# Performance work log

Measured on AMD Instinct MI355X. Metric: run time of the kernel, lower is better.

## Reference

```python
import jax, jax.numpy as jnp
import numpy as np

EPS = 1e-8
BOX2D_IDX = jnp.array([0, 1, 3, 4, 6])  # x, y, dx, dy, yaw


def box2corners(box):
    # box: (..., 5) = (x, y, w, h, alpha) -> corners (..., 4, 2), CCW order
    x, y, w, h, a = (box[..., i] for i in range(5))
    tx = jnp.array([0.5, -0.5, -0.5, 0.5], box.dtype)
    ty = jnp.array([0.5, 0.5, -0.5, -0.5], box.dtype)
    x4 = tx * w[..., None]
    y4 = ty * h[..., None]
    c, s = jnp.cos(a)[..., None], jnp.sin(a)[..., None]
    rx = c * x4 - s * y4 + x[..., None]
    ry = s * x4 + c * y4 + y[..., None]
    return jnp.stack([rx, ry], axis=-1)


def edge_intersections(c1, c2):
    # all 4x4 edge-edge intersections of two quads -> pts (..., 16, 2), mask (..., 16)
    p1 = c1[..., :, None, :]
    p2 = jnp.roll(c1, -1, axis=-2)[..., :, None, :]
    q1 = c2[..., None, :, :]
    q2 = jnp.roll(c2, -1, axis=-2)[..., None, :, :]
    r = p2 - p1
    s = q2 - q1
    denom = r[..., 0] * s[..., 1] - r[..., 1] * s[..., 0]
    safe = jnp.where(jnp.abs(denom) < EPS, 1.0, denom)
    qp = q1 - p1
    t = (qp[..., 0] * s[..., 1] - qp[..., 1] * s[..., 0]) / safe
    u = (qp[..., 0] * r[..., 1] - qp[..., 1] * r[..., 0]) / safe
    mask = (jnp.abs(denom) > EPS) & (t > 0) & (t < 1) & (u > 0) & (u < 1)
    pts = jnp.where(mask[..., None], p1 + t[..., None] * r, 0.0)
    lead = pts.shape[:-3]
    return pts.reshape(lead + (16, 2)), mask.reshape(lead + (16,))


def points_in_box(pts, corners):
    # pts (..., K, 2) inside rotated quad given by corners (..., 4, 2) -> (..., K) bool
    a = corners[..., 0:1, :]
    ab = corners[..., 1:2, :] - a
    ad = corners[..., 3:4, :] - a
    ap = pts - a
    pab = jnp.sum(ap * ab, -1)
    pad = jnp.sum(ap * ad, -1)
    nab = jnp.sum(ab * ab, -1)
    nad = jnp.sum(ad * ad, -1)
    return (pab > 0) & (pab < nab) & (pad > 0) & (pad < nad)


def masked_polygon_area(verts, mask):
    # verts (..., 24, 2) candidate vertices, mask (..., 24) validity
    m = mask.astype(verts.dtype)
    num = jnp.maximum(jnp.sum(m, -1, keepdims=True), 1.0)
    mean = jnp.sum(verts * m[..., None], -2, keepdims=True) / num[..., None]
    d = verts - mean  # centered (shoelace is translation-invariant)
    ang = jnp.arctan2(d[..., 1], d[..., 0])
    # push invalid vertices to the end with stable tie-break
    ang = jnp.where(mask, ang, 1e6 + jnp.arange(24, dtype=ang.dtype))
    idx = jnp.argsort(ang, axis=-1)
    vs = jnp.take_along_axis(d, idx[..., None], axis=-2)
    ms = jnp.take_along_axis(mask, idx, axis=-1)
    v0 = vs[..., 0:1, :]
    vs = jnp.where(ms[..., None], vs, v0)  # collapse invalid onto first vertex
    nxt = jnp.roll(vs, -1, axis=-2)
    cross = vs[..., 0] * nxt[..., 1] - vs[..., 1] * nxt[..., 0]
    return 0.5 * jnp.abs(jnp.sum(cross, -1))


def rotated_iou_3d(b1, b2):
    # b1, b2: (..., 7) = (x, y, z, dx, dy, dz, yaw); elementwise-aligned IoU
    c1 = box2corners(b1[..., BOX2D_IDX])
    c2 = box2corners(b2[..., BOX2D_IDX])
    ipts, imask = edge_intersections(c1, c2)
    in1 = points_in_box(c1, c2)
    in2 = points_in_box(c2, c1)
    verts = jnp.concatenate([c1, c2, ipts], axis=-2)  # (..., 24, 2)
    mask = jnp.concatenate([in1, in2, imask], axis=-1)
    inter2d = masked_polygon_area(verts, mask)
    zmax = jnp.minimum(b1[..., 2] + 0.5 * b1[..., 5], b2[..., 2] + 0.5 * b2[..., 5])
    zmin = jnp.maximum(b1[..., 2] - 0.5 * b1[..., 5], b2[..., 2] - 0.5 * b2[..., 5])
    inter3d = inter2d * jnp.maximum(zmax - zmin, 0.0)
    v1 = b1[..., 3] * b1[..., 4] * b1[..., 5]
    v2 = b2[..., 3] * b2[..., 4] * b2[..., 5]
    return inter3d / (v1 + v2 - inter3d + EPS)


def setup_inputs() -> dict:
    key = jax.random.key(0)
    k1, k2, k3, k4, k5 = jax.random.split(key, 5)
    N = 1048576
    ctr = (jax.random.uniform(k1, (N, 3)) - 0.5) * 40.0
    dims = jax.random.uniform(k2, (N, 3)) * 2.0 + 0.5
    yaw = (jax.random.uniform(k3, (N, 1)) - 0.5) * (2.0 * np.pi)
    pred = jnp.concatenate([ctr, dims, yaw], axis=-1).astype(jnp.float32)
    noise = jax.random.normal(k4, (N, 7)) * jnp.array(
        [0.3, 0.3, 0.3, 0.2, 0.2, 0.2, 0.2], jnp.float32)
    target = pred + noise
    target = target.at[:, 3:6].set(jnp.maximum(target[:, 3:6], 0.1))
    weight = jax.random.uniform(k5, (N,), dtype=jnp.float32)
    return {"pred": pred, "target": target, "weight": weight}


def reference(pred, target, weight):
    # IoU3DLoss(with_yaw=True, reduction='mean', loss_weight=1.0)
    loss_weight = 1.0
    iou = rotated_iou_3d(pred[None, ...], target[None, ...])  # (1, N)
    iou_loss = (1.0 - iou) * weight
    return loss_weight * jnp.mean(iou_loss)
```

## Files before the change

kernel.cpp:

```cpp
#include <hip/hip_runtime.h>

#define EPS_F 1e-8f
#define BLOCK 256
#define MAXGRID 2048

typedef float vf4 __attribute__((ext_vector_type(4)));

__device__ __forceinline__ vf4 load4u(const float* p) {
    vf4 v;
    __builtin_memcpy(&v, p, 16);
    return v;
}

__device__ __forceinline__ float fast_rcp(float x) {
    return __builtin_amdgcn_rcpf(x);
}

__device__ __forceinline__ void fast_sincos(float x, float* s, float* c) {
    float t = x * 0.15915494309189535f;
    t = __builtin_amdgcn_fractf(t);
    *s = __builtin_amdgcn_sinf(t);
    *c = __builtin_amdgcn_cosf(t);
}

__device__ __forceinline__ float edge_contrib(float ax, float ay,
                                              float bx, float by,
                                              float W, float H) {
    float dx = bx - ax, dy = by - ay;
    float sdx = (fabsf(dx) < 1e-20f) ? 1e-20f : dx;
    float sdy = (fabsf(dy) < 1e-20f) ? 1e-20f : dy;
    float rdx = fast_rcp(sdx);
    float rdy = fast_rcp(sdy);

    float tA = (-W - ax) * rdx;
    float tB = ( W - ax) * rdx;
    float ta = fmaxf(fminf(tA, tB), 0.f);
    float tb = fminf(fmaxf(tA, tB), 1.f);
    tb = fmaxf(ta, tb);

    float u0 = (-H - ay) * rdy;
    float u1 = ( H - ay) * rdy;
    float tm0 = fminf(u0, u1), tm1 = fmaxf(u0, u1);
    float t1 = fminf(fmaxf(tm0, ta), tb);
    float t2 = fminf(fmaxf(tm1, ta), tb);

    float x0 = fmaf(ta, dx, ax), y0 = fmaf(ta, dy, ay);
    float x1 = fmaf(t1, dx, ax), y1 = fmaf(t1, dy, ay);
    float x2 = fmaf(t2, dx, ax), y2 = fmaf(t2, dy, ay);
    float x3 = fmaf(tb, dx, ax), y3 = fmaf(tb, dy, ay);
    float h0 = fminf(fmaxf(y0, -H), H) + H;
    float h1 = fminf(fmaxf(y1, -H), H) + H;
    float h2 = fminf(fmaxf(y2, -H), H) + H;
    float h3 = fminf(fmaxf(y3, -H), H) + H;

    return (x1 - x0) * (h0 + h1) + (x2 - x1) * (h1 + h2) + (x3 - x2) * (h2 + h3);
}

__global__ __launch_bounds__(BLOCK, 8) void iou3d_partial_kernel(
    const float* __restrict__ pred, const float* __restrict__ target,
    const float* __restrict__ weight, float* __restrict__ partials,
    int N, int stride, int iters)
{
    int i = blockIdx.x * BLOCK + threadIdx.x;

    int j = (i < N) ? i : 0;
    long o = (long)j * 7;
    vf4 A0 = load4u(pred + o),  A1 = load4u(pred + o + 3);
    vf4 B0 = load4u(target + o), B1 = load4u(target + o + 3);
    float wg = (i < N) ? weight[j] : 0.f;

    float val = 0.f;
    #pragma unroll 1
    for (int it = 0; it < iters; ++it) {
        vf4 a0 = A0, a1 = A1, b0 = B0, b1 = B1;
        float w = wg;

        int inext = i + stride;
        if (it + 1 < iters) {
            int jn = (inext < N) ? inext : 0;
            long on = (long)jn * 7;
            A0 = load4u(pred + on);  A1 = load4u(pred + on + 3);
            B0 = load4u(target + on); B1 = load4u(target + on + 3);
            wg = (inext < N) ? weight[jn] : 0.f;
        }
        i = inext;

        float s1, c1, sd, cd;
        fast_sincos(a1.w, &s1, &c1);
        fast_sincos(b1.w - a1.w, &sd, &cd);
        float dxc = b0.x - a0.x, dyc = b0.y - a0.y;
        float tx =  c1 * dxc + s1 * dyc;
        float ty = -s1 * dxc + c1 * dyc;
        float W = 0.5f * a1.x, H = 0.5f * a1.y;
        float w2 = 0.5f * b1.x, h2 = 0.5f * b1.y;

        float cw = cd * w2, sw = sd * w2, ch = cd * h2, sh = sd * h2;
        float q0x =  cw - sh + tx, q0y =  sw + ch + ty;
        float q1x = -cw - sh + tx, q1y = -sw + ch + ty;
        float q2x = -cw + sh + tx, q2y = -sw - ch + ty;
        float q3x =  cw + sh + tx, q3y =  sw - ch + ty;

        float s  = edge_contrib(q0x, q0y, q1x, q1y, W, H)
                 + edge_contrib(q1x, q1y, q2x, q2y, W, H)
                 + edge_contrib(q2x, q2y, q3x, q3y, W, H)
                 + edge_contrib(q3x, q3y, q0x, q0y, W, H);
        float area = 0.5f * fabsf(s);

        float zmax = fminf(a0.z + 0.5f * a1.z, b0.z + 0.5f * b1.z);
        float zmin = fmaxf(a0.z - 0.5f * a1.z, b0.z - 0.5f * b1.z);
        float inter3d = area * fmaxf(zmax - zmin, 0.f);
        float v1 = a1.x * a1.y * a1.z;
        float v2 = b1.x * b1.y * b1.z;
        float iou = inter3d * fast_rcp(v1 + v2 - inter3d + EPS_F);
        val += (1.f - iou) * w;
    }

    #pragma unroll
    for (int off = 32; off > 0; off >>= 1) val += __shfl_down(val, off, 64);
    __shared__ float wsum[4];
    int lane = threadIdx.x & 63, wid = threadIdx.x >> 6;
    if (lane == 0) wsum[wid] = val;
    __syncthreads();
    if (threadIdx.x == 0)
        partials[blockIdx.x] = wsum[0] + wsum[1] + wsum[2] + wsum[3];
}

__global__ __launch_bounds__(BLOCK) void reduce_partials_kernel(
    const float* __restrict__ partials, float* __restrict__ out,
    int nparts, float invN)
{
    float v = 0.f;
    for (int k = threadIdx.x; k < nparts; k += BLOCK) v += partials[k];
    #pragma unroll
    for (int off = 32; off > 0; off >>= 1) v += __shfl_down(v, off, 64);
    __shared__ float wsum[4];
    int lane = threadIdx.x & 63, wid = threadIdx.x >> 6;
    if (lane == 0) wsum[wid] = v;
    __syncthreads();
    if (threadIdx.x == 0)
        out[0] = (wsum[0] + wsum[1] + wsum[2] + wsum[3]) * invN;
}

extern "C" void kernel_launch(void* const* d_in, const int* in_sizes, int n_in,
                              void* d_out, int out_size, void* d_ws, size_t ws_size,
                              hipStream_t stream) {
    const float* pred   = (const float*)d_in[0];
    const float* target = (const float*)d_in[1];
    const float* weight = (const float*)d_in[2];
    float* out = (float*)d_out;
    float* partials = (float*)d_ws;
    int N = in_sizes[2];

    int nblocks = (N + BLOCK - 1) / BLOCK;
    int grid = (nblocks < MAXGRID) ? nblocks : MAXGRID;
    int stride = grid * BLOCK;
    int iters = (N + stride - 1) / stride;

    iou3d_partial_kernel<<<grid, BLOCK, 0, stream>>>(pred, target, weight,
                                                     partials, N, stride, iters);
    reduce_partials_kernel<<<1, BLOCK, 0, stream>>>(partials, out, grid,
                                                    1.f / (float)N);
}
```

Before: 99.78 us.

## Stage coalesced box slabs through double-buffered LDS and share edge reciprocals

Replaces per-thread strided 7-float unaligned loads with block-wide coalesced 16-byte loads of pred/target slabs into a double-buffered shared-memory array, with register prefetch of the next slab overlapping compute. Exploits the rectangle's parallel edges so only two edge vectors and four reciprocals are computed per box pair instead of four and eight. Grid is halved to 1024 blocks with launch bounds lowered to 4, adding LDS usage and a barrier per iteration. Unaligned strided LDS reads (stride 7) may incur bank conflicts.

```diff
diff --git a/kernel.cpp b/kernel.cpp
--- a/kernel.cpp
+++ b/kernel.cpp
@@ -2,7 +2,8 @@
 
 #define EPS_F 1e-8f
 #define BLOCK 256
-#define MAXGRID 2048
+#define GRID  1024
+#define SLAB_CH 896
 
 typedef float vf4 __attribute__((ext_vector_type(4)));
 
@@ -24,14 +25,9 @@
 }
 
 __device__ __forceinline__ float edge_contrib(float ax, float ay,
-                                              float bx, float by,
+                                              float dx, float dy,
+                                              float rdx, float rdy,
                                               float W, float H) {
-    float dx = bx - ax, dy = by - ay;
-    float sdx = (fabsf(dx) < 1e-20f) ? 1e-20f : dx;
-    float sdy = (fabsf(dy) < 1e-20f) ? 1e-20f : dy;
-    float rdx = fast_rcp(sdx);
-    float rdy = fast_rcp(sdy);
-
     float tA = (-W - ax) * rdx;
     float tB = ( W - ax) * rdx;
     float ta = fmaxf(fminf(tA, tB), 0.f);
@@ -56,72 +52,143 @@
     return (x1 - x0) * (h0 + h1) + (x2 - x1) * (h1 + h2) + (x3 - x2) * (h2 + h3);
 }
 
-__global__ __launch_bounds__(BLOCK, 8) void iou3d_partial_kernel(
+__global__ __launch_bounds__(BLOCK, 4) void iou3d_partial_kernel(
     const float* __restrict__ pred, const float* __restrict__ target,
     const float* __restrict__ weight, float* __restrict__ partials,
-    int N, int stride, int iters)
+    int N, int stride_e, int iters)
 {
-    int i = blockIdx.x * BLOCK + threadIdx.x;
-
-    int j = (i < N) ? i : 0;
-    long o = (long)j * 7;
-    vf4 A0 = load4u(pred + o),  A1 = load4u(pred + o + 3);
-    vf4 B0 = load4u(target + o), B1 = load4u(target + o + 3);
-    float wg = (i < N) ? weight[j] : 0.f;
+    __shared__ vf4 lds4[2 * SLAB_CH];
+    const int tid = threadIdx.x;
+    const long maxdw = 7L * N - 4;
+
+
+    {
+        long g0 = (long)blockIdx.x * 256 * 7;
+        #pragma unroll
+        for (int k = 0; k < 4; ++k) {
+            int c = k * BLOCK + tid;
+            if (c < SLAB_CH) {
+                bool isP = (c < 448);
+                long gdw = g0 + 4L * c - (isP ? 0 : 1792);
+                gdw = (gdw > maxdw) ? maxdw : gdw;
+                lds4[c] = load4u((isP ? pred : target) + gdw);
+            }
+        }
+    }
+    int i0 = blockIdx.x * 256 + tid;
+    float wcur = (i0 < N) ? weight[i0] : 0.f;
+    __syncthreads();
 
     float val = 0.f;
     #pragma unroll 1
     for (int it = 0; it < iters; ++it) {
-        vf4 a0 = A0, a1 = A1, b0 = B0, b1 = B1;
-        float w = wg;
-
-        int inext = i + stride;
-        if (it + 1 < iters) {
-            int jn = (inext < N) ? inext : 0;
-            long on = (long)jn * 7;
-            A0 = load4u(pred + on);  A1 = load4u(pred + on + 3);
-            B0 = load4u(target + on); B1 = load4u(target + on + 3);
-            wg = (inext < N) ? weight[jn] : 0.f;
-        }
-        i = inext;
-
-        float s1, c1, sd, cd;
-        fast_sincos(a1.w, &s1, &c1);
-        fast_sincos(b1.w - a1.w, &sd, &cd);
-        float dxc = b0.x - a0.x, dyc = b0.y - a0.y;
-        float tx =  c1 * dxc + s1 * dyc;
-        float ty = -s1 * dxc + c1 * dyc;
-        float W = 0.5f * a1.x, H = 0.5f * a1.y;
-        float w2 = 0.5f * b1.x, h2 = 0.5f * b1.y;
-
-        float cw = cd * w2, sw = sd * w2, ch = cd * h2, sh = sd * h2;
-        float q0x =  cw - sh + tx, q0y =  sw + ch + ty;
-        float q1x = -cw - sh + tx, q1y = -sw + ch + ty;
-        float q2x = -cw + sh + tx, q2y = -sw - ch + ty;
-        float q3x =  cw + sh + tx, q3y =  sw - ch + ty;
-
-        float s  = edge_contrib(q0x, q0y, q1x, q1y, W, H)
-                 + edge_contrib(q1x, q1y, q2x, q2y, W, H)
-                 + edge_contrib(q2x, q2y, q3x, q3y, W, H)
-                 + edge_contrib(q3x, q3y, q0x, q0y, W, H);
-        float area = 0.5f * fabsf(s);
-
-        float zmax = fminf(a0.z + 0.5f * a1.z, b0.z + 0.5f * b1.z);
-        float zmin = fmaxf(a0.z - 0.5f * a1.z, b0.z - 0.5f * b1.z);
-        float inter3d = area * fmaxf(zmax - zmin, 0.f);
-        float v1 = a1.x * a1.y * a1.z;
-        float v2 = b1.x * b1.y * b1.z;
-        float iou = inter3d * fast_rcp(v1 + v2 - inter3d + EPS_F);
-        val += (1.f - iou) * w;
+        bool more = (it + 1 < iters);
+
+        vf4 R0, R1, R2, R3;
+        float wnext = 0.f;
+        if (more) {
+            long g0 = ((long)blockIdx.x * 256 + (long)(it + 1) * stride_e) * 7;
+            {
+                int c = tid;              long g = g0 + 4L * c;
+                g = (g > maxdw) ? maxdw : g;  R0 = load4u(pred + g);
+            }
+            {
+                int c = BLOCK + tid;      long g = g0 + 4L * c;
+                g = (g > maxdw) ? maxdw : g;  R1 = load4u(pred + g);
+            }
+            {
+                int c = 2 * BLOCK + tid;  long g = g0 + 4L * c - 1792;
+                g = (g > maxdw) ? maxdw : g;  R2 = load4u(target + g);
+            }
+            {
+                int c = 3 * BLOCK + tid;
+                long g = g0 + 4L * c - 1792;
+                g = (g < 0) ? 0 : ((g > maxdw) ? maxdw : g);
+                R3 = load4u(target + g);
+            }
+            int inext = blockIdx.x * 256 + (it + 1) * stride_e + tid;
+            wnext = (inext < N) ? weight[inext] : 0.f;
+        }
+
+        if (more) {
+            int c = BLOCK + tid;
+            if (c >= 448) {
+                long g0 = ((long)blockIdx.x * 256 + (long)(it + 1) * stride_e) * 7;
+                long g = g0 + 4L * c - 1792;
+                g = (g > maxdw) ? maxdw : g;
+                R1 = load4u(target + g);
+            }
+        }
+
+        {
+            const float* ldsf = (const float*)(lds4 + (it & 1) * 0);
+            const float* base = (const float*)lds4;
+            const float* p;
+            const float* q;
+            p = base + (size_t)(it & 1) * (SLAB_CH * 4) + 7 * tid;
+            q = p + 1792;
+            (void)ldsf;
+
+            float a0 = p[0], a1 = p[1], a2 = p[2], a3 = p[3], a4 = p[4], a5 = p[5], a6 = p[6];
+            float b0 = q[0], b1 = q[1], b2 = q[2], b3 = q[3], b4 = q[4], b5 = q[5], b6 = q[6];
+
+            float s1, c1, sd, cd;
+            fast_sincos(a6, &s1, &c1);
+            fast_sincos(b6 - a6, &sd, &cd);
+            float dxc = b0 - a0, dyc = b1 - a1;
+            float tx =  c1 * dxc + s1 * dyc;
+            float ty = -s1 * dxc + c1 * dyc;
+            float W = 0.5f * a3, H = 0.5f * a4;
+            float w2 = 0.5f * b3, h2 = 0.5f * b4;
+
+            float cw = cd * w2, sw = sd * w2, ch = cd * h2, sh = sd * h2;
+            float q0x =  cw - sh + tx, q0y =  sw + ch + ty;
+            float q1x = -cw - sh + tx, q1y = -sw + ch + ty;
+            float q2x = -cw + sh + tx, q2y = -sw - ch + ty;
+            float q3x =  cw + sh + tx, q3y =  sw - ch + ty;
+
+            float e0x = -2.f * cw, e0y = -2.f * sw;
+            float e1x =  2.f * sh, e1y = -2.f * ch;
+            float g0x = (fabsf(e0x) < 1e-20f) ? 1e-20f : e0x;
+            float g0y = (fabsf(e0y) < 1e-20f) ? 1e-20f : e0y;
+            float g1x = (fabsf(e1x) < 1e-20f) ? 1e-20f : e1x;
+            float g1y = (fabsf(e1y) < 1e-20f) ? 1e-20f : e1y;
+            float r0x = fast_rcp(g0x), r0y = fast_rcp(g0y);
+            float r1x = fast_rcp(g1x), r1y = fast_rcp(g1y);
+
+            float s = edge_contrib(q0x, q0y,  e0x,  e0y,  r0x,  r0y, W, H)
+                    + edge_contrib(q1x, q1y,  e1x,  e1y,  r1x,  r1y, W, H)
+                    + edge_contrib(q2x, q2y, -e0x, -e0y, -r0x, -r0y, W, H)
+                    + edge_contrib(q3x, q3y, -e1x, -e1y, -r1x, -r1y, W, H);
+            float area = 0.5f * fabsf(s);
+
+            float zmax = fminf(a2 + 0.5f * a5, b2 + 0.5f * b5);
+            float zmin = fmaxf(a2 - 0.5f * a5, b2 - 0.5f * b5);
+            float inter3d = area * fmaxf(zmax - zmin, 0.f);
+            float v1 = a3 * a4 * a5;
+            float v2 = b3 * b4 * b5;
+            float iou = inter3d * fast_rcp(v1 + v2 - inter3d + EPS_F);
+            val += (1.f - iou) * wcur;
+        }
+
+        if (more) {
+            vf4* dst = lds4 + ((it + 1) & 1) * SLAB_CH;
+            dst[tid]             = R0;
+            dst[BLOCK + tid]     = R1;
+            dst[2 * BLOCK + tid] = R2;
+            if (3 * BLOCK + tid < SLAB_CH) dst[3 * BLOCK + tid] = R3;
+        }
+        __syncthreads();
+        wcur = wnext;
     }
 
     #pragma unroll
     for (int off = 32; off > 0; off >>= 1) val += __shfl_down(val, off, 64);
     __shared__ float wsum[4];
-    int lane = threadIdx.x & 63, wid = threadIdx.x >> 6;
+    int lane = tid & 63, wid = tid >> 6;
     if (lane == 0) wsum[wid] = val;
     __syncthreads();
-    if (threadIdx.x == 0)
+    if (tid == 0)
         partials[blockIdx.x] = wsum[0] + wsum[1] + wsum[2] + wsum[3];
 }
 
@@ -152,12 +219,12 @@
     int N = in_sizes[2];
 
     int nblocks = (N + BLOCK - 1) / BLOCK;
-    int grid = (nblocks < MAXGRID) ? nblocks : MAXGRID;
-    int stride = grid * BLOCK;
-    int iters = (N + stride - 1) / stride;
+    int grid = (nblocks < GRID) ? nblocks : GRID;
+    int stride_e = grid * BLOCK;
+    int iters = (N + stride_e - 1) / stride_e;
 
     iou3d_partial_kernel<<<grid, BLOCK, 0, stream>>>(pred, target, weight,
-                                                     partials, N, stride, iters);
+                                                     partials, N, stride_e, iters);
     reduce_partials_kernel<<<1, BLOCK, 0, stream>>>(partials, out, grid,
                                                     1.f / (float)N);
 }
```

After: 98.42 us. About the same (-1.4%).
